# Kernel tuning notes

Measured on AMD Instinct MI355X. Metric: run time of the kernel, lower is better.

The kernel has to match this reference:

```python
import jax, jax.numpy as jnp
import numpy as np

N_NODES = 10000
N_EDGES = 160000
IN_CH = 1030
HID = 256
HEADS = 4
OUT_CH = 49
NEG_SLOPE = 0.2
EPS = 1e-5


def setup_inputs() -> dict:
    key = jax.random.key(0)
    ks = jax.random.split(key, 20)
    HC = HID * HEADS  # 1024
    inp = {
        "x": jax.random.normal(ks[0], (N_NODES, IN_CH), dtype=jnp.float32),
        "edge_index": jax.random.randint(ks[1], (2, N_EDGES), 0, N_NODES, dtype=jnp.int64),
        # conv1 (GATv2): lin_l (source), lin_r (target), att, out bias
        "c1_wl": jax.random.normal(ks[2], (IN_CH, HC), dtype=jnp.float32) * 0.03,
        "c1_bl": jnp.zeros((HC,), dtype=jnp.float32),
        "c1_wr": jax.random.normal(ks[3], (IN_CH, HC), dtype=jnp.float32) * 0.03,
        "c1_br": jnp.zeros((HC,), dtype=jnp.float32),
        "c1_att": jax.random.normal(ks[4], (HEADS, HID), dtype=jnp.float32) * 0.06,
        "c1_bias": jnp.zeros((HC,), dtype=jnp.float32),
        # norm1 (per-node LayerNorm over channels)
        "ln1_w": jnp.ones((HC,), dtype=jnp.float32),
        "ln1_b": jnp.zeros((HC,), dtype=jnp.float32),
        # conv2
        "c2_wl": jax.random.normal(ks[5], (HC, HC), dtype=jnp.float32) * 0.03,
        "c2_bl": jnp.zeros((HC,), dtype=jnp.float32),
        "c2_wr": jax.random.normal(ks[6], (HC, HC), dtype=jnp.float32) * 0.03,
        "c2_br": jnp.zeros((HC,), dtype=jnp.float32),
        "c2_att": jax.random.normal(ks[7], (HEADS, HID), dtype=jnp.float32) * 0.06,
        "c2_bias": jnp.zeros((HC,), dtype=jnp.float32),
        # norm2
        "ln2_w": jnp.ones((HC,), dtype=jnp.float32),
        "ln2_b": jnp.zeros((HC,), dtype=jnp.float32),
        # classifier: Linear(HC, HID) -> ELU -> Linear(HID, OUT_CH)
        "cls_w1": jax.random.normal(ks[8], (HC, HID), dtype=jnp.float32) * 0.03,
        "cls_b1": jnp.zeros((HID,), dtype=jnp.float32),
        "cls_w2": jax.random.normal(ks[9], (HID, OUT_CH), dtype=jnp.float32) * 0.06,
        "cls_b2": jnp.zeros((OUT_CH,), dtype=jnp.float32),
    }
    return inp


def gatv2_conv(x, src, dst, wl, bl, wr, br, att, bias, n_nodes):
    """PyG GATv2Conv, concat heads. src/dst include self loops."""
    H, C = att.shape
    xl = (x @ wl + bl).reshape(-1, H, C)  # source transform [N,H,C]
    xr = (x @ wr + br).reshape(-1, H, C)  # target transform [N,H,C]
    m = xl[src] + xr[dst]                  # [E,H,C] gather + add
    e = jnp.einsum("ehc,hc->eh", jax.nn.leaky_relu(m, NEG_SLOPE), att)  # [E,H]
    # segment softmax over destination node
    emax = jax.ops.segment_max(e, dst, num_segments=n_nodes)
    p = jnp.exp(e - emax[dst])
    denom = jax.ops.segment_sum(p, dst, num_segments=n_nodes)
    alpha = p / (denom[dst] + 1e-16)       # [E,H]
    out = jax.ops.segment_sum(xl[src] * alpha[:, :, None], dst, num_segments=n_nodes)
    return out.reshape(n_nodes, H * C) + bias


def layer_norm(x, w, b):
    mu = jnp.mean(x, axis=-1, keepdims=True)
    var = jnp.var(x, axis=-1, keepdims=True)
    return (x - mu) / jnp.sqrt(var + EPS) * w + b


def reference(x, edge_index, c1_wl, c1_bl, c1_wr, c1_br, c1_att, c1_bias,
              ln1_w, ln1_b, c2_wl, c2_bl, c2_wr, c2_br, c2_att, c2_bias,
              ln2_w, ln2_b, cls_w1, cls_b1, cls_w2, cls_b2):
    n = x.shape[0]
    loops = jnp.arange(n, dtype=edge_index.dtype)
    src = jnp.concatenate([edge_index[0], loops])  # add_self_loops=True
    dst = jnp.concatenate([edge_index[1], loops])

    h = gatv2_conv(x, src, dst, c1_wl, c1_bl, c1_wr, c1_br, c1_att, c1_bias, n)
    h = jax.nn.elu(layer_norm(h, ln1_w, ln1_b))
    # dropout: identity at inference
    h = gatv2_conv(h, src, dst, c2_wl, c2_bl, c2_wr, c2_br, c2_att, c2_bias, n)
    h = jax.nn.elu(layer_norm(h, ln2_w, ln2_b))
    h = jax.nn.elu(h @ cls_w1 + cls_b1)
    return h @ cls_w2 + cls_b2  # [N, 49]
```

## Files before the change

kernel.cpp:

```cpp
#include <hip/hip_runtime.h>
#include <stdint.h>

#define N_NODES 10000
#define N_EDGES 160000
#define E_TOT   170000
#define IN_CH   1030
#define HC      1024
#define OUT_CH  49
#define NEG_SLOPE 0.2f
#define LN_EPS 1e-5f
#define LOG2E 1.4426950408889634f

#define MPAD  10112
#define K1PAD 1088

typedef __attribute__((ext_vector_type(8))) __bf16 bf16x8;
typedef __attribute__((ext_vector_type(4))) float floatx4;
typedef __attribute__((ext_vector_type(2))) float floatx2;
typedef _Float16 h2 __attribute__((ext_vector_type(2)));

static __device__ __forceinline__ unsigned short f2bf(float f) {
  union { float f; uint32_t u; } v; v.f = f;
  uint32_t u = v.u;
  u += 0x7fffu + ((u >> 16) & 1u);
  return (unsigned short)(u >> 16);
}
static __device__ __forceinline__ unsigned short f2h(float f) {
  _Float16 h = (_Float16)f;
  union { _Float16 h; unsigned short u; } v; v.h = h; return v.u;
}
static __device__ __forceinline__ h2 bits2h2(uint32_t u) {
  union { uint32_t i; h2 h; } v; v.i = u; return v.h;
}
static __device__ __forceinline__ floatx2 h2f2(h2 a) {
  floatx2 r; r.x = (float)a.x; r.y = (float)a.y; return r;
}

static __device__ __forceinline__ float wred_add(float x) {
#define DPP_ADD(ctrl, rmask)                                                   \
  x += __builtin_bit_cast(float, __builtin_amdgcn_update_dpp(                  \
           0, __builtin_bit_cast(int, x), ctrl, rmask, 0xf, true))
  DPP_ADD(0x111, 0xf);
  DPP_ADD(0x112, 0xf);
  DPP_ADD(0x114, 0xf);
  DPP_ADD(0x118, 0xf);
  DPP_ADD(0x142, 0xa);
  DPP_ADD(0x143, 0xc);
#undef DPP_ADD
  return __builtin_bit_cast(float,
      __builtin_amdgcn_readlane(__builtin_bit_cast(int, x), 63));
}


__global__ void cast_x_kernel(const float* __restrict__ x, unsigned short* __restrict__ xa,
                              int* __restrict__ counts, int* __restrict__ cursor) {
  int idx = blockIdx.x * 256 + threadIdx.x;
  if (idx < N_NODES) { counts[idx] = 0; cursor[idx] = 0; }
  if (idx >= N_NODES * K1PAD) return;
  int m = idx / K1PAD, k = idx - m * K1PAD;
  float v = (k < IN_CH) ? x[m * IN_CH + k] : 0.f;
  xa[idx] = f2bf(v);
}

__global__ void transpose_cast_kernel(const float* __restrict__ wa, const float* __restrict__ wb,
                                      int split, int lda, int ldb,
                                      int Kvalid, int Kout, unsigned short* __restrict__ out) {
  __shared__ float tile[32][33];
  int n0 = blockIdx.x * 32, k0 = blockIdx.y * 32;
  int tx = threadIdx.x, ty = threadIdx.y;
#pragma unroll
  for (int i = 0; i < 4; i++) {
    int k = k0 + ty + i * 8;
    int n = n0 + tx;
    float v = 0.f;
    if (k < Kvalid) v = (n < split) ? wa[(size_t)k * lda + n] : wb[(size_t)k * ldb + (n - split)];
    tile[ty + i * 8][tx] = v;
  }
  __syncthreads();
#pragma unroll
  for (int i = 0; i < 4; i++) {
    int n = n0 + ty + i * 8;
    int k = k0 + tx;
    out[(size_t)n * Kout + k] = f2bf(tile[tx][ty + i * 8]);
  }
}


__global__ void count_kernel(const int* __restrict__ dstArr, int* __restrict__ counts) {
  int e = blockIdx.x * 256 + threadIdx.x;
  if (e >= E_TOT) return;
  int d = (e < N_EDGES) ? dstArr[e] : (e - N_EDGES);
  atomicAdd(&counts[d], 1);
}

__global__ __launch_bounds__(256) void scan_kernel(const int* __restrict__ counts,
                                                   int* __restrict__ rstart) {
  __shared__ int sm[256];
  int t = threadIdx.x;
  int b0 = t * 40;
  int b1 = b0 + 40; if (b1 > N_NODES) b1 = N_NODES; if (b0 > N_NODES) b0 = N_NODES;
  int s = 0;
  for (int i = b0; i < b1; i++) s += counts[i];
  sm[t] = s; __syncthreads();
  for (int st = 1; st < 256; st <<= 1) {
    int add = (t >= st) ? sm[t - st] : 0;
    __syncthreads();
    sm[t] += add;
    __syncthreads();
  }
  int run = sm[t] - s;
  for (int i = b0; i < b1; i++) { rstart[i] = run; run += counts[i]; }
  if (t == 255) rstart[N_NODES] = run;
}

__global__ void scatter_kernel(const int* __restrict__ srcArr, const int* __restrict__ dstArr,
                               const int* __restrict__ row_start,
                               int* __restrict__ cursor, int* __restrict__ csrsrc) {
  int e = blockIdx.x * 256 + threadIdx.x;
  if (e >= E_TOT) {
    return;
  }
  if (e < 16) csrsrc[E_TOT + e] = 0;
  int d, sv;
  if (e < N_EDGES) { d = dstArr[e]; sv = srcArr[e]; }
  else { d = e - N_EDGES; sv = d; }
  int pos = atomicAdd(&cursor[d], 1);
  csrsrc[row_start[d] + pos] = sv;
}

template <int MODE, int KC>
__global__ __launch_bounds__(256, 4) void gemm_bf16(
    const unsigned short* __restrict__ A, const unsigned short* __restrict__ Bt,
    float* __restrict__ Cf, unsigned short* __restrict__ Cb,
    const float* __restrict__ blo, const float* __restrict__ bhi,
    int M, int ldc, int bsplit)
{
  __shared__ __align__(16) unsigned short As[128 * 64];
  __shared__ __align__(16) unsigned short Bs[128 * 64];
  const int t = threadIdx.x;
  const int w = t >> 6, lane = t & 63;

  const unsigned int nwg = gridDim.x * gridDim.y;
  const unsigned int bid = blockIdx.y * gridDim.x + blockIdx.x;
  const unsigned int q8 = nwg >> 3, r8 = nwg & 7;
  const unsigned int xcd = bid & 7, sub = bid >> 3;
  const unsigned int wg = (xcd < r8 ? xcd * (q8 + 1) : r8 * (q8 + 1) + (xcd - r8) * q8) + sub;
  const int tile_n = (wg % gridDim.x) * 128, tile_m = (wg / gridDim.x) * 128;

  floatx4 acc[4][4] = {};

  const int qq = w * 64 + lane;
  const int row0 = qq >> 3;
  const int gj = (qq & 7) ^ (row0 & 7);
  const unsigned short* gA0 = A  + (size_t)(tile_m + row0) * KC + gj * 8;
  const unsigned short* gB0 = Bt + (size_t)(tile_n + row0) * KC + gj * 8;

  const int wm = (w >> 1) * 64, wn = (w & 1) * 64;
  const int lrow = lane & 15, cg0 = (lane >> 4);
  const int sw = lrow & 7;

#pragma unroll 1
  for (int k0 = 0; k0 < KC; k0 += 64) {
#pragma unroll
    for (int p = 0; p < 4; p++) {
      __builtin_amdgcn_global_load_lds(
          (const __attribute__((address_space(1))) void*)(gA0 + p * 32 * KC),
          (__attribute__((address_space(3))) void*)(As + p * 2048 + w * 512), 16, 0, 0);
      __builtin_amdgcn_global_load_lds(
          (const __attribute__((address_space(1))) void*)(gB0 + p * 32 * KC),
          (__attribute__((address_space(3))) void*)(Bs + p * 2048 + w * 512), 16, 0, 0);
    }
    gA0 += 64; gB0 += 64;
    __syncthreads();
#pragma unroll
    for (int h = 0; h < 2; h++) {
      const int sc = (h * 4 + cg0) ^ sw;
      bf16x8 a[4], b[4];
#pragma unroll
      for (int mi = 0; mi < 4; mi++)
        a[mi] = *(const bf16x8*)(As + (wm + mi * 16 + lrow) * 64 + sc * 8);
#pragma unroll
      for (int ni = 0; ni < 4; ni++)
        b[ni] = *(const bf16x8*)(Bs + (wn + ni * 16 + lrow) * 64 + sc * 8);
#pragma unroll
      for (int mi = 0; mi < 4; mi++)
#pragma unroll
        for (int ni = 0; ni < 4; ni++)
          acc[mi][ni] = __builtin_amdgcn_mfma_f32_16x16x32_bf16(a[mi], b[ni], acc[mi][ni], 0, 0, 0);
    }
    __syncthreads();
  }

  const int rbase = (lane >> 4) * 4;
#pragma unroll
  for (int mi = 0; mi < 4; mi++) {
#pragma unroll
    for (int r = 0; r < 4; r++) {
      int m = tile_m + wm + mi * 16 + rbase + r;
      if (m >= M) continue;
#pragma unroll
      for (int ni = 0; ni < 4; ni++) {
        int n = tile_n + wn + ni * 16 + lrow;
        float v = acc[mi][ni][r] + (n < bsplit ? blo[n] : bhi[n - bsplit]);
        if (MODE == 0) {
          Cf[(size_t)m * ldc + n] = v;
        } else if (MODE == 1) {
          Cf[(size_t)m * ldc + n] = v > 0.f ? v : expm1f(v);
        } else {
          Cb[(size_t)m * 2048 + n] = f2h(v);
        }
      }
    }
  }
}


__global__ __launch_bounds__(256) void gat_ln_kernel(
    const unsigned short* __restrict__ xlr,
    const float* __restrict__ att,
    const int* __restrict__ csrsrc, const int* __restrict__ rstart,
    const float* __restrict__ bias,
    const float* __restrict__ lnw, const float* __restrict__ lnb,
    unsigned short* __restrict__ out)
{
  const int d = blockIdx.x;
  const int t = threadIdx.x;
  const int lane = t & 63, wv = t >> 6;
  const int c = wv * 256 + lane * 4;

  uint2 xru = *(const uint2*)(xlr + (size_t)d * 2048 + 1024 + c);
  h2 xr0 = bits2h2(xru.x), xr1 = bits2h2(xru.y);
  float4 aw4 = *(const float4*)(att + c);
  h2 aw0, aw1;
  aw0.x = (_Float16)(aw4.x * LOG2E); aw0.y = (_Float16)(aw4.y * LOG2E);
  aw1.x = (_Float16)(aw4.z * LOG2E); aw1.y = (_Float16)(aw4.w * LOG2E);
  const h2 ns = {(_Float16)NEG_SLOPE, (_Float16)NEG_SLOPE};
  const unsigned short* xbase = xlr + c;

  int start = rstart[d], deg = rstart[d + 1] - start;

  float m = -3.0e38f, l = 0.f;
  floatx2 accA = {0.f, 0.f}, accB = {0.f, 0.f};

  int i = 0;
  if (deg >= 4) {
    int sA0 = csrsrc[start],     sA1 = csrsrc[start + 1];
    int sA2 = csrsrc[start + 2], sA3 = csrsrc[start + 3];
    uint2 uA0 = *(const uint2*)(xbase + (size_t)sA0 * 2048);
    uint2 uA1 = *(const uint2*)(xbase + (size_t)sA1 * 2048);
    uint2 uA2 = *(const uint2*)(xbase + (size_t)sA2 * 2048);
    uint2 uA3 = *(const uint2*)(xbase + (size_t)sA3 * 2048);
    int sB0 = csrsrc[start + 4], sB1 = csrsrc[start + 5];
    int sB2 = csrsrc[start + 6], sB3 = csrsrc[start + 7];
    for (; i + 4 <= deg; i += 4) {
      int sC0 = csrsrc[start + i + 8],  sC1 = csrsrc[start + i + 9];
      int sC2 = csrsrc[start + i + 10], sC3 = csrsrc[start + i + 11];
      uint2 uB0 = *(const uint2*)(xbase + (size_t)sB0 * 2048);
      uint2 uB1 = *(const uint2*)(xbase + (size_t)sB1 * 2048);
      uint2 uB2 = *(const uint2*)(xbase + (size_t)sB2 * 2048);
      uint2 uB3 = *(const uint2*)(xbase + (size_t)sB3 * 2048);

      h2 xh0a = bits2h2(uA0.x), xh0b = bits2h2(uA0.y);
      h2 xh1a = bits2h2(uA1.x), xh1b = bits2h2(uA1.y);
      h2 xh2a = bits2h2(uA2.x), xh2b = bits2h2(uA2.y);
      h2 xh3a = bits2h2(uA3.x), xh3b = bits2h2(uA3.y);
      h2 t0a = xh0a + xr0, t0b = xh0b + xr1;
      h2 t1a = xh1a + xr0, t1b = xh1b + xr1;
      h2 t2a = xh2a + xr0, t2b = xh2b + xr1;
      h2 t3a = xh3a + xr0, t3b = xh3b + xr1;
      h2 r0a = __builtin_elementwise_max(t0a, t0a * ns);
      h2 r0b = __builtin_elementwise_max(t0b, t0b * ns);
      h2 r1a = __builtin_elementwise_max(t1a, t1a * ns);
      h2 r1b = __builtin_elementwise_max(t1b, t1b * ns);
      h2 r2a = __builtin_elementwise_max(t2a, t2a * ns);
      h2 r2b = __builtin_elementwise_max(t2b, t2b * ns);
      h2 r3a = __builtin_elementwise_max(t3a, t3a * ns);
      h2 r3b = __builtin_elementwise_max(t3b, t3b * ns);
      float p0 = __builtin_amdgcn_fdot2(r0b, aw1, __builtin_amdgcn_fdot2(r0a, aw0, 0.f, false), false);
      float p1 = __builtin_amdgcn_fdot2(r1b, aw1, __builtin_amdgcn_fdot2(r1a, aw0, 0.f, false), false);
      float p2 = __builtin_amdgcn_fdot2(r2b, aw1, __builtin_amdgcn_fdot2(r2a, aw0, 0.f, false), false);
      float p3 = __builtin_amdgcn_fdot2(r3b, aw1, __builtin_amdgcn_fdot2(r3a, aw0, 0.f, false), false);
      p0 = wred_add(p0);
      p1 = wred_add(p1);
      p2 = wred_add(p2);
      p3 = wred_add(p3);
      float mx = fmaxf(fmaxf(p0, p1), fmaxf(p2, p3));
      if (mx > m) {
        float sc = exp2f(m - mx);
        floatx2 scv; scv.x = sc; scv.y = sc;
        accA *= scv; accB *= scv; l *= sc;
        m = mx;
      }
      float pe0 = exp2f(p0 - m), pe1 = exp2f(p1 - m);
      float pe2 = exp2f(p2 - m), pe3 = exp2f(p3 - m);
      floatx2 x0A = h2f2(xh0a), x0B = h2f2(xh0b);
      floatx2 x1A = h2f2(xh1a), x1B = h2f2(xh1b);
      floatx2 x2A = h2f2(xh2a), x2B = h2f2(xh2b);
      floatx2 x3A = h2f2(xh3a), x3B = h2f2(xh3b);
      floatx2 v0; v0.x = pe0; v0.y = pe0;
      floatx2 v1; v1.x = pe1; v1.y = pe1;
      floatx2 v2; v2.x = pe2; v2.y = pe2;
      floatx2 v3; v3.x = pe3; v3.y = pe3;
      accA += x0A * v0; accA += x1A * v1; accA += x2A * v2; accA += x3A * v3;
      accB += x0B * v0; accB += x1B * v1; accB += x2B * v2; accB += x3B * v3;
      l += pe0 + pe1 + pe2 + pe3;

      uA0 = uB0; uA1 = uB1; uA2 = uB2; uA3 = uB3;
      sB0 = sC0; sB1 = sC1; sB2 = sC2; sB3 = sC3;
    }
  }
  for (; i < deg; i++) {
    int s0 = csrsrc[start + i];
    uint2 u0 = *(const uint2*)(xbase + (size_t)s0 * 2048);
    h2 xh0a = bits2h2(u0.x), xh0b = bits2h2(u0.y);
    h2 t0a = xh0a + xr0, t0b = xh0b + xr1;
    h2 r0a = __builtin_elementwise_max(t0a, t0a * ns);
    h2 r0b = __builtin_elementwise_max(t0b, t0b * ns);
    float p0 = __builtin_amdgcn_fdot2(r0b, aw1, __builtin_amdgcn_fdot2(r0a, aw0, 0.f, false), false);
    p0 = wred_add(p0);
    if (p0 > m) {
      float sc = exp2f(m - p0);
      floatx2 scv; scv.x = sc; scv.y = sc;
      accA *= scv; accB *= scv; l *= sc;
      m = p0;
    }
    float pe0 = exp2f(p0 - m);
    floatx2 x0A = h2f2(xh0a), x0B = h2f2(xh0b);
    floatx2 pe0v; pe0v.x = pe0; pe0v.y = pe0;
    accA += x0A * pe0v;
    accB += x0B * pe0v;
    l += pe0;
  }

  float rd = 1.f / (l + 1e-16f);
  float4 bv = *(const float4*)(bias + c);
  float o0 = accA.x * rd + bv.x, o1 = accA.y * rd + bv.y;
  float o2 = accB.x * rd + bv.z, o3 = accB.y * rd + bv.w;

  __shared__ float ws1[4], ws2[4];
  float s1 = o0 + o1 + o2 + o3;
  float s2 = o0 * o0 + o1 * o1 + o2 * o2 + o3 * o3;
#pragma unroll
  for (int mm = 32; mm >= 1; mm >>= 1) {
    s1 += __shfl_xor(s1, mm, 64);
    s2 += __shfl_xor(s2, mm, 64);
  }
  if (lane == 0) { ws1[wv] = s1; ws2[wv] = s2; }
  __syncthreads();
  float mean = (ws1[0] + ws1[1] + ws1[2] + ws1[3]) * (1.f / 1024.f);
  float var  = (ws2[0] + ws2[1] + ws2[2] + ws2[3]) * (1.f / 1024.f) - mean * mean;
  float rstd = rsqrtf(var + LN_EPS);
  float4 wv4 = *(const float4*)(lnw + c);
  float4 bb  = *(const float4*)(lnb + c);
  float z0 = (o0 - mean) * rstd * wv4.x + bb.x; z0 = z0 > 0.f ? z0 : expm1f(z0);
  float z1 = (o1 - mean) * rstd * wv4.y + bb.y; z1 = z1 > 0.f ? z1 : expm1f(z1);
  float z2 = (o2 - mean) * rstd * wv4.z + bb.z; z2 = z2 > 0.f ? z2 : expm1f(z2);
  float z3 = (o3 - mean) * rstd * wv4.w + bb.w; z3 = z3 > 0.f ? z3 : expm1f(z3);
  ushort4 u;
  u.x = f2bf(z0); u.y = f2bf(z1); u.z = f2bf(z2); u.w = f2bf(z3);
  *(ushort4*)(out + (size_t)d * 1024 + c) = u;
}


__global__ __launch_bounds__(64) void cls2_kernel(
    const float* __restrict__ h3, const float* __restrict__ w2,
    const float* __restrict__ b2, float* __restrict__ out)
{
  __shared__ float row[256];
  int node = blockIdx.x, t = threadIdx.x;
  *(float4*)(row + t * 4) = *(const float4*)(h3 + (size_t)node * 256 + t * 4);
  __syncthreads();
  if (t < OUT_CH) {
    float a0 = 0.f, a1 = 0.f, a2 = 0.f, a3 = 0.f;
#pragma unroll 4
    for (int k = 0; k < 256; k += 4) {
      float4 r = *(const float4*)(row + k);
      a0 += r.x * w2[(k + 0) * OUT_CH + t];
      a1 += r.y * w2[(k + 1) * OUT_CH + t];
      a2 += r.z * w2[(k + 2) * OUT_CH + t];
      a3 += r.w * w2[(k + 3) * OUT_CH + t];
    }
    out[node * OUT_CH + t] = (a0 + a1) + (a2 + a3) + b2[t];
  }
}


extern "C" void kernel_launch(void* const* d_in, const int* in_sizes, int n_in,
                              void* d_out, int out_size, void* d_ws, size_t ws_size,
                              hipStream_t stream)
{
  const float* x       = (const float*)d_in[0];
  const int*   ei      = (const int*)d_in[1];
  const float* c1_wl   = (const float*)d_in[2];
  const float* c1_bl   = (const float*)d_in[3];
  const float* c1_wr   = (const float*)d_in[4];
  const float* c1_br   = (const float*)d_in[5];
  const float* c1_att  = (const float*)d_in[6];
  const float* c1_bias = (const float*)d_in[7];
  const float* ln1_w   = (const float*)d_in[8];
  const float* ln1_b   = (const float*)d_in[9];
  const float* c2_wl   = (const float*)d_in[10];
  const float* c2_bl   = (const float*)d_in[11];
  const float* c2_wr   = (const float*)d_in[12];
  const float* c2_br   = (const float*)d_in[13];
  const float* c2_att  = (const float*)d_in[14];
  const float* c2_bias = (const float*)d_in[15];
  const float* ln2_w   = (const float*)d_in[16];
  const float* ln2_b   = (const float*)d_in[17];
  const float* cls_w1  = (const float*)d_in[18];
  const float* cls_b1  = (const float*)d_in[19];
  const float* cls_w2  = (const float*)d_in[20];
  const float* cls_b2  = (const float*)d_in[21];

  const int* srcArr = ei;
  const int* dstArr = ei + N_EDGES;

  char* ws = (char*)d_ws;
  size_t off = 0;
  auto alloc = [&](size_t bytes) { void* p = ws + off; off += (bytes + 255) & ~(size_t)255; return p; };
  unsigned short* xa      = (unsigned short*)alloc((size_t)MPAD * K1PAD * 2);
  unsigned short* wt1     = (unsigned short*)alloc((size_t)2048 * K1PAD * 2);
  unsigned short* wt2     = (unsigned short*)alloc((size_t)2048 * 1024 * 2);
  unsigned short* wtc1    = (unsigned short*)alloc((size_t)256 * 1024 * 2);
  unsigned short* xlr     = (unsigned short*)alloc((size_t)N_NODES * 2048 * 2);
  float*          h3      = (float*)alloc((size_t)N_NODES * 256 * 4);
  unsigned short* hb      = (unsigned short*)alloc((size_t)MPAD * 1024 * 2);
  int*            counts  = (int*)alloc(N_NODES * 4);
  int*            cursor  = (int*)alloc(N_NODES * 4);
  int*            rstart  = (int*)alloc((N_NODES + 1) * 4);
  int*            csrsrc  = (int*)alloc((E_TOT + 16) * 4);
  (void)in_sizes; (void)n_in; (void)out_size; (void)ws_size;

  cast_x_kernel<<<(N_NODES * K1PAD + 255) / 256, 256, 0, stream>>>(x, xa, counts, cursor);
  transpose_cast_kernel<<<dim3(64, 34), dim3(32, 8), 0, stream>>>(c1_wl, c1_wr, 1024, 1024, 1024, IN_CH, K1PAD, wt1);
  transpose_cast_kernel<<<dim3(64, 32), dim3(32, 8), 0, stream>>>(c2_wl, c2_wr, 1024, 1024, 1024, 1024, 1024, wt2);
  transpose_cast_kernel<<<dim3(8, 32), dim3(32, 8), 0, stream>>>(cls_w1, cls_w1, 256, 256, 256, 1024, 1024, wtc1);

  count_kernel<<<(E_TOT + 255) / 256, 256, 0, stream>>>(dstArr, counts);
  scan_kernel<<<1, 256, 0, stream>>>(counts, rstart);
  scatter_kernel<<<(E_TOT + 255) / 256, 256, 0, stream>>>(srcArr, dstArr, rstart, cursor, csrsrc);

  gemm_bf16<2, K1PAD><<<dim3(16, 79), 256, 0, stream>>>(xa, wt1, nullptr, xlr, c1_bl, c1_br, N_NODES, 0, 1024);
  gat_ln_kernel<<<N_NODES, 256, 0, stream>>>(xlr, c1_att, csrsrc, rstart, c1_bias, ln1_w, ln1_b, hb);

  gemm_bf16<2, 1024><<<dim3(16, 79), 256, 0, stream>>>(hb, wt2, nullptr, xlr, c2_bl, c2_br, N_NODES, 0, 1024);
  gat_ln_kernel<<<N_NODES, 256, 0, stream>>>(xlr, c2_att, csrsrc, rstart, c2_bias, ln2_w, ln2_b, hb);

  gemm_bf16<1, 1024><<<dim3(2, 79), 256, 0, stream>>>(hb, wtc1, h3, nullptr, cls_b1, cls_b1, N_NODES, 256, 1024);
  cls2_kernel<<<N_NODES, 64, 0, stream>>>(h3, cls_w2, cls_b2, (float*)d_out);
}
```

Baseline: 481.9 us.

## Merge weight transposes and edge counting into one prep kernel, simplify CSR build

Folds the three weight transpose-cast launches and the edge count kernel into a single block-indexed prep kernel, cutting launch count and letting the small jobs run side by side. The scan now writes a working copy of row starts so the scatter can atomically bump it directly, which removes the separate cursor array. The GAT aggregation loop drops its scalar tail and handles partial groups of four with clamped indices and masked exponentials. This keeps one uniform unrolled loop at the cost of some redundant loads for the last group.

Measured after the change: 498.3 us. 3.4% more time.

```diff
diff --git a/kernel.cpp b/kernel.cpp
--- a/kernel.cpp
+++ b/kernel.cpp
@@ -53,21 +53,21 @@
 
 
 __global__ void cast_x_kernel(const float* __restrict__ x, unsigned short* __restrict__ xa,
-                              int* __restrict__ counts, int* __restrict__ cursor) {
+                              int* __restrict__ counts) {
   int idx = blockIdx.x * 256 + threadIdx.x;
-  if (idx < N_NODES) { counts[idx] = 0; cursor[idx] = 0; }
+  if (idx < N_NODES) counts[idx] = 0;
   if (idx >= N_NODES * K1PAD) return;
   int m = idx / K1PAD, k = idx - m * K1PAD;
   float v = (k < IN_CH) ? x[m * IN_CH + k] : 0.f;
   xa[idx] = f2bf(v);
 }
 
-__global__ void transpose_cast_kernel(const float* __restrict__ wa, const float* __restrict__ wb,
-                                      int split, int lda, int ldb,
-                                      int Kvalid, int Kout, unsigned short* __restrict__ out) {
-  __shared__ float tile[32][33];
-  int n0 = blockIdx.x * 32, k0 = blockIdx.y * 32;
-  int tx = threadIdx.x, ty = threadIdx.y;
+static __device__ __forceinline__ void transpose_body(
+    float (*tile)[33], const float* __restrict__ wa, const float* __restrict__ wb,
+    int split, int lda, int ldb, int Kvalid, int Kout,
+    unsigned short* __restrict__ out, int bx, int by, int t) {
+  int n0 = bx * 32, k0 = by * 32;
+  int tx = t & 31, ty = t >> 5;
 #pragma unroll
   for (int i = 0; i < 4; i++) {
     int k = k0 + ty + i * 8;
@@ -85,16 +85,40 @@
   }
 }
 
-
-__global__ void count_kernel(const int* __restrict__ dstArr, int* __restrict__ counts) {
-  int e = blockIdx.x * 256 + threadIdx.x;
-  if (e >= E_TOT) return;
-  int d = (e < N_EDGES) ? dstArr[e] : (e - N_EDGES);
-  atomicAdd(&counts[d], 1);
+#define NB_W1 2176
+#define NB_W2 2048
+#define NB_WC 256
+#define NB_CNT 665
+__global__ __launch_bounds__(256) void prep2_kernel(
+    const float* __restrict__ c1_wl, const float* __restrict__ c1_wr,
+    const float* __restrict__ c2_wl, const float* __restrict__ c2_wr,
+    const float* __restrict__ cls_w1,
+    const int* __restrict__ dstArr, int* __restrict__ counts,
+    unsigned short* __restrict__ wt1, unsigned short* __restrict__ wt2,
+    unsigned short* __restrict__ wtc1)
+{
+  __shared__ float tile[32][33];
+  int b = blockIdx.x, t = threadIdx.x;
+  if (b < NB_W1) {
+    transpose_body(tile, c1_wl, c1_wr, 1024, 1024, 1024, IN_CH, K1PAD, wt1, b & 63, b >> 6, t);
+  } else if (b < NB_W1 + NB_W2) {
+    int bb = b - NB_W1;
+    transpose_body(tile, c2_wl, c2_wr, 1024, 1024, 1024, 1024, 1024, wt2, bb & 63, bb >> 6, t);
+  } else if (b < NB_W1 + NB_W2 + NB_WC) {
+    int bb = b - (NB_W1 + NB_W2);
+    transpose_body(tile, cls_w1, cls_w1, 256, 256, 256, 1024, 1024, wtc1, bb & 7, bb >> 3, t);
+  } else {
+    int e = (b - (NB_W1 + NB_W2 + NB_WC)) * 256 + t;
+    if (e < E_TOT) {
+      int d = (e < N_EDGES) ? dstArr[e] : (e - N_EDGES);
+      atomicAdd(&counts[d], 1);
+    }
+  }
 }
 
 __global__ __launch_bounds__(256) void scan_kernel(const int* __restrict__ counts,
-                                                   int* __restrict__ rstart) {
+                                                   int* __restrict__ rstart,
+                                                   int* __restrict__ rwork) {
   __shared__ int sm[256];
   int t = threadIdx.x;
   int b0 = t * 40;
@@ -109,23 +133,19 @@
     __syncthreads();
   }
   int run = sm[t] - s;
-  for (int i = b0; i < b1; i++) { rstart[i] = run; run += counts[i]; }
+  for (int i = b0; i < b1; i++) { rstart[i] = run; rwork[i] = run; run += counts[i]; }
   if (t == 255) rstart[N_NODES] = run;
 }
 
 __global__ void scatter_kernel(const int* __restrict__ srcArr, const int* __restrict__ dstArr,
-                               const int* __restrict__ row_start,
-                               int* __restrict__ cursor, int* __restrict__ csrsrc) {
+                               int* __restrict__ rwork, int* __restrict__ csrsrc) {
   int e = blockIdx.x * 256 + threadIdx.x;
-  if (e >= E_TOT) {
-    return;
-  }
-  if (e < 16) csrsrc[E_TOT + e] = 0;
+  if (e >= E_TOT) return;
   int d, sv;
   if (e < N_EDGES) { d = dstArr[e]; sv = srcArr[e]; }
   else { d = e - N_EDGES; sv = d; }
-  int pos = atomicAdd(&cursor[d], 1);
-  csrsrc[row_start[d] + pos] = sv;
+  int pos = atomicAdd(&rwork[d], 1);
+  csrsrc[pos] = sv;
 }
 
 template <int MODE, int KC>
@@ -237,100 +257,83 @@
   const h2 ns = {(_Float16)NEG_SLOPE, (_Float16)NEG_SLOPE};
   const unsigned short* xbase = xlr + c;
 
-  int start = rstart[d], deg = rstart[d + 1] - start;
+  const int start = rstart[d], end = rstart[d + 1];
+  const int last = end - 1;
+  const int ngroups = (end - start + 3) >> 2;
 
   float m = -3.0e38f, l = 0.f;
   floatx2 accA = {0.f, 0.f}, accB = {0.f, 0.f};
 
-  int i = 0;
-  if (deg >= 4) {
-    int sA0 = csrsrc[start],     sA1 = csrsrc[start + 1];
-    int sA2 = csrsrc[start + 2], sA3 = csrsrc[start + 3];
-    uint2 uA0 = *(const uint2*)(xbase + (size_t)sA0 * 2048);
-    uint2 uA1 = *(const uint2*)(xbase + (size_t)sA1 * 2048);
-    uint2 uA2 = *(const uint2*)(xbase + (size_t)sA2 * 2048);
-    uint2 uA3 = *(const uint2*)(xbase + (size_t)sA3 * 2048);
-    int sB0 = csrsrc[start + 4], sB1 = csrsrc[start + 5];
-    int sB2 = csrsrc[start + 6], sB3 = csrsrc[start + 7];
-    for (; i + 4 <= deg; i += 4) {
-      int sC0 = csrsrc[start + i + 8],  sC1 = csrsrc[start + i + 9];
-      int sC2 = csrsrc[start + i + 10], sC3 = csrsrc[start + i + 11];
-      uint2 uB0 = *(const uint2*)(xbase + (size_t)sB0 * 2048);
-      uint2 uB1 = *(const uint2*)(xbase + (size_t)sB1 * 2048);
-      uint2 uB2 = *(const uint2*)(xbase + (size_t)sB2 * 2048);
-      uint2 uB3 = *(const uint2*)(xbase + (size_t)sB3 * 2048);
-
-      h2 xh0a = bits2h2(uA0.x), xh0b = bits2h2(uA0.y);
-      h2 xh1a = bits2h2(uA1.x), xh1b = bits2h2(uA1.y);
-      h2 xh2a = bits2h2(uA2.x), xh2b = bits2h2(uA2.y);
-      h2 xh3a = bits2h2(uA3.x), xh3b = bits2h2(uA3.y);
-      h2 t0a = xh0a + xr0, t0b = xh0b + xr1;
-      h2 t1a = xh1a + xr0, t1b = xh1b + xr1;
-      h2 t2a = xh2a + xr0, t2b = xh2b + xr1;
-      h2 t3a = xh3a + xr0, t3b = xh3b + xr1;
-      h2 r0a = __builtin_elementwise_max(t0a, t0a * ns);
-      h2 r0b = __builtin_elementwise_max(t0b, t0b * ns);
-      h2 r1a = __builtin_elementwise_max(t1a, t1a * ns);
-      h2 r1b = __builtin_elementwise_max(t1b, t1b * ns);
-      h2 r2a = __builtin_elementwise_max(t2a, t2a * ns);
-      h2 r2b = __builtin_elementwise_max(t2b, t2b * ns);
-      h2 r3a = __builtin_elementwise_max(t3a, t3a * ns);
-      h2 r3b = __builtin_elementwise_max(t3b, t3b * ns);
-      float p0 = __builtin_amdgcn_fdot2(r0b, aw1, __builtin_amdgcn_fdot2(r0a, aw0, 0.f, false), false);
-      float p1 = __builtin_amdgcn_fdot2(r1b, aw1, __builtin_amdgcn_fdot2(r1a, aw0, 0.f, false), false);
-      float p2 = __builtin_amdgcn_fdot2(r2b, aw1, __builtin_amdgcn_fdot2(r2a, aw0, 0.f, false), false);
-      float p3 = __builtin_amdgcn_fdot2(r3b, aw1, __builtin_amdgcn_fdot2(r3a, aw0, 0.f, false), false);
-      p0 = wred_add(p0);
-      p1 = wred_add(p1);
-      p2 = wred_add(p2);
-      p3 = wred_add(p3);
-      float mx = fmaxf(fmaxf(p0, p1), fmaxf(p2, p3));
-      if (mx > m) {
-        float sc = exp2f(m - mx);
-        floatx2 scv; scv.x = sc; scv.y = sc;
-        accA *= scv; accB *= scv; l *= sc;
-        m = mx;
-      }
-      float pe0 = exp2f(p0 - m), pe1 = exp2f(p1 - m);
-      float pe2 = exp2f(p2 - m), pe3 = exp2f(p3 - m);
-      floatx2 x0A = h2f2(xh0a), x0B = h2f2(xh0b);
-      floatx2 x1A = h2f2(xh1a), x1B = h2f2(xh1b);
-      floatx2 x2A = h2f2(xh2a), x2B = h2f2(xh2b);
-      floatx2 x3A = h2f2(xh3a), x3B = h2f2(xh3b);
-      floatx2 v0; v0.x = pe0; v0.y = pe0;
-      floatx2 v1; v1.x = pe1; v1.y = pe1;
-      floatx2 v2; v2.x = pe2; v2.y = pe2;
-      floatx2 v3; v3.x = pe3; v3.y = pe3;
-      accA += x0A * v0; accA += x1A * v1; accA += x2A * v2; accA += x3A * v3;
-      accB += x0B * v0; accB += x1B * v1; accB += x2B * v2; accB += x3B * v3;
-      l += pe0 + pe1 + pe2 + pe3;
-
-      uA0 = uB0; uA1 = uB1; uA2 = uB2; uA3 = uB3;
-      sB0 = sC0; sB1 = sC1; sB2 = sC2; sB3 = sC3;
-    }
-  }
-  for (; i < deg; i++) {
-    int s0 = csrsrc[start + i];
-    uint2 u0 = *(const uint2*)(xbase + (size_t)s0 * 2048);
-    h2 xh0a = bits2h2(u0.x), xh0b = bits2h2(u0.y);
+#define CIDX(e) csrsrc[(e) < last ? (e) : last]
+  int sA0 = CIDX(start),     sA1 = CIDX(start + 1);
+  int sA2 = CIDX(start + 2), sA3 = CIDX(start + 3);
+  uint2 uA0 = *(const uint2*)(xbase + (size_t)sA0 * 2048);
+  uint2 uA1 = *(const uint2*)(xbase + (size_t)sA1 * 2048);
+  uint2 uA2 = *(const uint2*)(xbase + (size_t)sA2 * 2048);
+  uint2 uA3 = *(const uint2*)(xbase + (size_t)sA3 * 2048);
+  int sB0 = CIDX(start + 4), sB1 = CIDX(start + 5);
+  int sB2 = CIDX(start + 6), sB3 = CIDX(start + 7);
+
+  for (int g = 0; g < ngroups; g++) {
+    const int base = start + (g << 2);
+    int sC0 = CIDX(base + 8),  sC1 = CIDX(base + 9);
+    int sC2 = CIDX(base + 10), sC3 = CIDX(base + 11);
+    uint2 uB0 = *(const uint2*)(xbase + (size_t)sB0 * 2048);
+    uint2 uB1 = *(const uint2*)(xbase + (size_t)sB1 * 2048);
+    uint2 uB2 = *(const uint2*)(xbase + (size_t)sB2 * 2048);
+    uint2 uB3 = *(const uint2*)(xbase + (size_t)sB3 * 2048);
+
+    h2 xh0a = bits2h2(uA0.x), xh0b = bits2h2(uA0.y);
+    h2 xh1a = bits2h2(uA1.x), xh1b = bits2h2(uA1.y);
+    h2 xh2a = bits2h2(uA2.x), xh2b = bits2h2(uA2.y);
+    h2 xh3a = bits2h2(uA3.x), xh3b = bits2h2(uA3.y);
     h2 t0a = xh0a + xr0, t0b = xh0b + xr1;
+    h2 t1a = xh1a + xr0, t1b = xh1b + xr1;
+    h2 t2a = xh2a + xr0, t2b = xh2b + xr1;
+    h2 t3a = xh3a + xr0, t3b = xh3b + xr1;
     h2 r0a = __builtin_elementwise_max(t0a, t0a * ns);
     h2 r0b = __builtin_elementwise_max(t0b, t0b * ns);
+    h2 r1a = __builtin_elementwise_max(t1a, t1a * ns);
+    h2 r1b = __builtin_elementwise_max(t1b, t1b * ns);
+    h2 r2a = __builtin_elementwise_max(t2a, t2a * ns);
+    h2 r2b = __builtin_elementwise_max(t2b, t2b * ns);
+    h2 r3a = __builtin_elementwise_max(t3a, t3a * ns);
+    h2 r3b = __builtin_elementwise_max(t3b, t3b * ns);
     float p0 = __builtin_amdgcn_fdot2(r0b, aw1, __builtin_amdgcn_fdot2(r0a, aw0, 0.f, false), false);
+    float p1 = __builtin_amdgcn_fdot2(r1b, aw1, __builtin_amdgcn_fdot2(r1a, aw0, 0.f, false), false);
+    float p2 = __builtin_amdgcn_fdot2(r2b, aw1, __builtin_amdgcn_fdot2(r2a, aw0, 0.f, false), false);
+    float p3 = __builtin_amdgcn_fdot2(r3b, aw1, __builtin_amdgcn_fdot2(r3a, aw0, 0.f, false), false);
     p0 = wred_add(p0);
-    if (p0 > m) {
-      float sc = exp2f(m - p0);
+    p1 = wred_add(p1);
+    p2 = wred_add(p2);
+    p3 = wred_add(p3);
+    float mx = fmaxf(fmaxf(p0, p1), fmaxf(p2, p3));
+    if (mx > m) {
+      float sc = exp2f(m - mx);
       floatx2 scv; scv.x = sc; scv.y = sc;
       accA *= scv; accB *= scv; l *= sc;
-      m = p0;
+      m = mx;
     }
     float pe0 = exp2f(p0 - m);
+    float pe1 = (base + 1 <= last) ? exp2f(p1 - m) : 0.f;
+    float pe2 = (base + 2 <= last) ? exp2f(p2 - m) : 0.f;
+    float pe3 = (base + 3 <= last) ? exp2f(p3 - m) : 0.f;
     floatx2 x0A = h2f2(xh0a), x0B = h2f2(xh0b);
-    floatx2 pe0v; pe0v.x = pe0; pe0v.y = pe0;
-    accA += x0A * pe0v;
-    accB += x0B * pe0v;
-    l += pe0;
-  }
+    floatx2 x1A = h2f2(xh1a), x1B = h2f2(xh1b);
+    floatx2 x2A = h2f2(xh2a), x2B = h2f2(xh2b);
+    floatx2 x3A = h2f2(xh3a), x3B = h2f2(xh3b);
+    floatx2 v0; v0.x = pe0; v0.y = pe0;
+    floatx2 v1; v1.x = pe1; v1.y = pe1;
+    floatx2 v2; v2.x = pe2; v2.y = pe2;
+    floatx2 v3; v3.x = pe3; v3.y = pe3;
+    accA += x0A * v0; accA += x1A * v1; accA += x2A * v2; accA += x3A * v3;
+    accB += x0B * v0; accB += x1B * v1; accB += x2B * v2; accB += x3B * v3;
+    l += pe0 + pe1 + pe2 + pe3;
+
+    uA0 = uB0; uA1 = uB1; uA2 = uB2; uA3 = uB3;
+    sB0 = sC0; sB1 = sC1; sB2 = sC2; sB3 = sC3;
+  }
+#undef CIDX
 
   float rd = 1.f / (l + 1e-16f);
   float4 bv = *(const float4*)(bias + c);
@@ -426,19 +429,17 @@
   float*          h3      = (float*)alloc((size_t)N_NODES * 256 * 4);
   unsigned short* hb      = (unsigned short*)alloc((size_t)MPAD * 1024 * 2);
   int*            counts  = (int*)alloc(N_NODES * 4);
-  int*            cursor  = (int*)alloc(N_NODES * 4);
+  int*            rwork   = (int*)alloc(N_NODES * 4);
   int*            rstart  = (int*)alloc((N_NODES + 1) * 4);
-  int*            csrsrc  = (int*)alloc((E_TOT + 16) * 4);
+  int*            csrsrc  = (int*)alloc(E_TOT * 4);
   (void)in_sizes; (void)n_in; (void)out_size; (void)ws_size;
 
-  cast_x_kernel<<<(N_NODES * K1PAD + 255) / 256, 256, 0, stream>>>(x, xa, counts, cursor);
-  transpose_cast_kernel<<<dim3(64, 34), dim3(32, 8), 0, stream>>>(c1_wl, c1_wr, 1024, 1024, 1024, IN_CH, K1PAD, wt1);
-  transpose_cast_kernel<<<dim3(64, 32), dim3(32, 8), 0, stream>>>(c2_wl, c2_wr, 1024, 1024, 1024, 1024, 1024, wt2);
-  transpose_cast_kernel<<<dim3(8, 32), dim3(32, 8), 0, stream>>>(cls_w1, cls_w1, 256, 256, 256, 1024, 1024, wtc1);
-
-  count_kernel<<<(E_TOT + 255) / 256, 256, 0, stream>>>(dstArr, counts);
-  scan_kernel<<<1, 256, 0, stream>>>(counts, rstart);
-  scatter_kernel<<<(E_TOT + 255) / 256, 256, 0, stream>>>(srcArr, dstArr, rstart, cursor, csrsrc);
+  cast_x_kernel<<<(N_NODES * K1PAD + 255) / 256, 256, 0, stream>>>(x, xa, counts);
+  prep2_kernel<<<NB_W1 + NB_W2 + NB_WC + NB_CNT, 256, 0, stream>>>(
+      c1_wl, c1_wr, c2_wl, c2_wr, cls_w1, dstArr, counts, wt1, wt2, wtc1);
+
+  scan_kernel<<<1, 256, 0, stream>>>(counts, rstart, rwork);
+  scatter_kernel<<<(E_TOT + 255) / 256, 256, 0, stream>>>(srcArr, dstArr, rwork, csrsrc);
 
   gemm_bf16<2, K1PAD><<<dim3(16, 79), 256, 0, stream>>>(xa, wt1, nullptr, xlr, c1_bl, c1_br, N_NODES, 0, 1024);
   gat_ln_kernel<<<N_NODES, 256, 0, stream>>>(xlr, c1_att, csrsrc, rstart, c1_bias, ln1_w, ln1_b, hb);
```
